# Optimization experiments

Measured on AMD Instinct MI355X. Metric: run time of the kernel, lower is better.

Reference implementation:

```python
import jax, jax.numpy as jnp
import numpy as np

N = 50000
E = 800000
IN_C = 128
HID = 64
HEADS = 4
OUT_C = 64
NEG_SLOPE = 0.2


def _glorot(key, shape):
    fan = shape[0] + shape[-1]
    return jax.random.normal(key, shape, dtype=jnp.float32) * jnp.sqrt(2.0 / fan)


def setup_inputs() -> dict:
    key = jax.random.key(0)
    ks = jax.random.split(key, 12)
    x = jax.random.normal(ks[0], (N, IN_C), dtype=jnp.float32)
    edge_index = jax.random.randint(ks[1], (2, E), 0, N, dtype=jnp.int64)
    edge_attr = jax.random.normal(ks[2], (E, 8), dtype=jnp.float32)
    # gat1: in -> heads*hid
    W1 = _glorot(ks[3], (IN_C, HEADS * HID))
    att_src1 = _glorot(ks[4], (HEADS, HID))
    att_dst1 = _glorot(ks[5], (HEADS, HID))
    b1 = jnp.zeros((HEADS * HID,), dtype=jnp.float32)
    # gat2: heads*hid -> out, 1 head
    W2 = _glorot(ks[6], (HEADS * HID, OUT_C))
    att_src2 = _glorot(ks[7], (1, OUT_C))
    att_dst2 = _glorot(ks[8], (1, OUT_C))
    b2 = jnp.zeros((OUT_C,), dtype=jnp.float32)
    return {"x": x, "edge_index": edge_index, "edge_attr": edge_attr,
            "W1": W1, "att_src1": att_src1, "att_dst1": att_dst1, "b1": b1,
            "W2": W2, "att_src2": att_src2, "att_dst2": att_dst2, "b2": b2}


def _gat_conv(x, src, dst, W, att_src, att_dst, b, heads, n_nodes):
    # x: [N, Cin] -> h: [N, H, C]
    h = (x @ W).reshape(n_nodes, heads, -1)
    a_src = jnp.sum(h * att_src, axis=-1)  # [N, H]
    a_dst = jnp.sum(h * att_dst, axis=-1)  # [N, H]
    e = jax.nn.leaky_relu(a_src[src] + a_dst[dst], NEG_SLOPE)  # [Etot, H]
    # segment softmax over destination node (self-loops guarantee non-empty segments)
    m = jax.ops.segment_max(e, dst, num_segments=n_nodes)      # [N, H]
    w = jnp.exp(e - m[dst])
    denom = jax.ops.segment_sum(w, dst, num_segments=n_nodes)  # [N, H]
    alpha = w / (denom[dst] + 1e-16)                           # [Etot, H]
    out = jax.ops.segment_sum(alpha[:, :, None] * h[src], dst, num_segments=n_nodes)
    return out.reshape(n_nodes, -1) + b  # concat heads (identity when heads==1)


def reference(x, edge_index, edge_attr, W1, att_src1, att_dst1, b1, W2, att_src2, att_dst2, b2):
    # PyG GATConv with edge_dim=None ignores edge_attr; add_self_loops=True by default.
    loop = jnp.arange(N, dtype=edge_index.dtype)
    src = jnp.concatenate([edge_index[0], loop])
    dst = jnp.concatenate([edge_index[1], loop])
    h = jax.nn.elu(_gat_conv(x, src, dst, W1, att_src1, att_dst1, b1, HEADS, N))
    out = jax.nn.elu(_gat_conv(h, src, dst, W2, att_src2, att_dst2, b2, 1, N))
    return out
```

## Files before the change

### kernel.cpp

```cpp
#include <hip/hip_runtime.h>
#include <hip/hip_bf16.h>
#include <math.h>

#define LEAKY 0.2f

#define BM 64
#define BN 64
#define BK 32
__global__ __launch_bounds__(256) void gemm_att(const float* __restrict__ A,
                                                const float* __restrict__ B,
                                                float* __restrict__ C,
                                                const float* __restrict__ att_s,
                                                const float* __restrict__ att_d,
                                                float* __restrict__ asrc,
                                                float* __restrict__ adst,
                                                int M, int K, int NC) {
    __shared__ float As[BK][BM + 1];
    __shared__ float Bs[BK][BN];
    const int tid = threadIdx.x;
    const int bm = blockIdx.x * BM;
    const int bn = blockIdx.y * BN;
    const int tx = tid & 15, ty = tid >> 4;
    float acc[4][4] = {};
    for (int k0 = 0; k0 < K; k0 += BK) {
        #pragma unroll
        for (int i = 0; i < (BM * BK) / 256; ++i) {
            int idx = tid + i * 256;
            int r = idx >> 5, c = idx & 31;
            int gr = bm + r;
            As[c][r] = (gr < M) ? A[(size_t)gr * K + k0 + c] : 0.f;
        }
        #pragma unroll
        for (int i = 0; i < (BK * BN) / 256; ++i) {
            int idx = tid + i * 256;
            int r = idx >> 6, c = idx & 63;
            Bs[r][c] = B[(size_t)(k0 + r) * NC + bn + c];
        }
        __syncthreads();
        #pragma unroll
        for (int k = 0; k < BK; ++k) {
            float a[4], b[4];
            #pragma unroll
            for (int i = 0; i < 4; ++i) a[i] = As[k][ty * 4 + i];
            #pragma unroll
            for (int j = 0; j < 4; ++j) b[j] = Bs[k][tx * 4 + j];
            #pragma unroll
            for (int i = 0; i < 4; ++i)
                #pragma unroll
                for (int j = 0; j < 4; ++j)
                    acc[i][j] += a[i] * b[j];
        }
        __syncthreads();
    }
    float s_att[4], d_att[4];
    #pragma unroll
    for (int j = 0; j < 4; ++j) {
        s_att[j] = att_s[bn + tx * 4 + j];
        d_att[j] = att_d[bn + tx * 4 + j];
    }
    const int head = bn >> 6;
    const int H = NC >> 6;
    #pragma unroll
    for (int i = 0; i < 4; ++i) {
        int gr = bm + ty * 4 + i;
        float ps = 0.f, pd = 0.f;
        #pragma unroll
        for (int j = 0; j < 4; ++j) {
            ps += acc[i][j] * s_att[j];
            pd += acc[i][j] * d_att[j];
        }
        #pragma unroll
        for (int o = 1; o < 16; o <<= 1) {
            ps += __shfl_xor(ps, o);
            pd += __shfl_xor(pd, o);
        }
        if (gr < M) {
            #pragma unroll
            for (int j = 0; j < 4; ++j)
                C[(size_t)gr * NC + bn + tx * 4 + j] = acc[i][j];
            if (tx == 0) {
                asrc[gr * H + head] = ps;
                adst[gr * H + head] = pd;
            }
        }
    }
}

__global__ __launch_bounds__(256) void count_deg(const int* __restrict__ ei, int E_, int N_,
                                                 int* __restrict__ deg) {
    int eid = blockIdx.x * 256 + threadIdx.x;
    int Etot = E_ + N_;
    if (eid >= Etot) return;
    int dst = (eid < E_) ? ei[E_ + eid] : (eid - E_);
    atomicAdd(&deg[dst], 1);
}

__global__ __launch_bounds__(1024) void scan_offsets(const int* __restrict__ deg,
                                                     int* __restrict__ off, int n) {
    __shared__ int wsum[16];
    int tid = threadIdx.x;
    int lane = tid & 63, w = tid >> 6;
    int chunk = (n + 1023) / 1024;
    int b = tid * chunk;
    int e = min(b + chunk, n);
    int s = 0;
    for (int i = b; i < e; ++i) s += deg[i];
    int v = s;
    #pragma unroll
    for (int o = 1; o < 64; o <<= 1) {
        int t = __shfl_up(v, o);
        if (lane >= o) v += t;
    }
    if (lane == 63) wsum[w] = v;
    __syncthreads();
    if (w == 0) {
        int t = (lane < 16) ? wsum[lane] : 0;
        #pragma unroll
        for (int o = 1; o < 16; o <<= 1) {
            int u = __shfl_up(t, o);
            if (lane >= o) t += u;
        }
        if (lane < 16) wsum[lane] = t;
    }
    __syncthreads();
    int acc = (w > 0 ? wsum[w - 1] : 0) + (v - s);
    for (int i = b; i < e; ++i) { off[i] = acc; acc += deg[i]; }
    if (e == n) off[n] = acc;
}

__global__ __launch_bounds__(256) void scatter_edges(const int* __restrict__ ei, int E_, int N_,
                                                     int* __restrict__ off,
                                                     int* __restrict__ csr) {
    int eid = blockIdx.x * 256 + threadIdx.x;
    int Etot = E_ + N_;
    if (eid >= Etot) return;
    int src, dst;
    if (eid < E_) { src = ei[eid]; dst = ei[E_ + eid]; }
    else          { src = dst = eid - E_; }
    int pos = atomicAdd(&off[dst], 1);
    csr[pos] = src;
}

__global__ __launch_bounds__(256) void gat_agg_h4(const int* __restrict__ off,
                                                  const int* __restrict__ csr,
                                                  const float* __restrict__ asrc,
                                                  const float* __restrict__ adst,
                                                  const float* __restrict__ hsrc,
                                                  const float* __restrict__ bias,
                                                  float* __restrict__ outp, int N_) {
    __shared__ float wls[4][256];
    __shared__ int   uls[4][64];
    int wv = threadIdx.x >> 6, lane = threadIdx.x & 63;
    int node = blockIdx.x * 4 + wv;
    if (node >= N_) return;
    int s = node ? off[node - 1] : 0;
    int e = off[node];
    int deg = e - s;
    float4 ad = *(const float4*)(adst + node * 4);
    float* wl = wls[wv];
    int*   ul = uls[wv];
    float a0 = 0.f, a1 = 0.f, a2 = 0.f, a3 = 0.f;
    float d0 = 0.f, d1 = 0.f, d2 = 0.f, d3 = 0.f;

    if (deg <= 64) {
        float e0 = -INFINITY, e1 = -INFINITY, e2 = -INFINITY, e3 = -INFINITY;
        int u = 0;
        if (lane < deg) {
            u = csr[s + lane];
            float4 as = *(const float4*)(asrc + u * 4);
            e0 = as.x + ad.x; e0 = e0 > 0.f ? e0 : LEAKY * e0;
            e1 = as.y + ad.y; e1 = e1 > 0.f ? e1 : LEAKY * e1;
            e2 = as.z + ad.z; e2 = e2 > 0.f ? e2 : LEAKY * e2;
            e3 = as.w + ad.w; e3 = e3 > 0.f ? e3 : LEAKY * e3;
        }
        float m0 = e0, m1 = e1, m2 = e2, m3 = e3;
        #pragma unroll
        for (int o = 32; o > 0; o >>= 1) {
            m0 = fmaxf(m0, __shfl_xor(m0, o));
            m1 = fmaxf(m1, __shfl_xor(m1, o));
            m2 = fmaxf(m2, __shfl_xor(m2, o));
            m3 = fmaxf(m3, __shfl_xor(m3, o));
        }
        if (lane < deg) {
            float w0 = __expf(e0 - m0), w1 = __expf(e1 - m1);
            float w2 = __expf(e2 - m2), w3 = __expf(e3 - m3);
            d0 = w0; d1 = w1; d2 = w2; d3 = w3;
            wl[lane] = w0; wl[64 + lane] = w1; wl[128 + lane] = w2; wl[192 + lane] = w3;
            ul[lane] = u;
        }
        int j = 0;
        for (; j + 2 <= deg; j += 2) {
            int u0 = ul[j], u1 = ul[j + 1];
            float W00 = wl[j],     W01 = wl[64 + j],     W02 = wl[128 + j],     W03 = wl[192 + j];
            float W10 = wl[j + 1], W11 = wl[64 + j + 1], W12 = wl[128 + j + 1], W13 = wl[192 + j + 1];
            const float* hp0 = hsrc + (size_t)u0 * 256 + lane;
            const float* hp1 = hsrc + (size_t)u1 * 256 + lane;
            float g00 = hp0[0], g01 = hp0[64], g02 = hp0[128], g03 = hp0[192];
            float g10 = hp1[0], g11 = hp1[64], g12 = hp1[128], g13 = hp1[192];
            a0 += W00 * g00; a1 += W01 * g01; a2 += W02 * g02; a3 += W03 * g03;
            a0 += W10 * g10; a1 += W11 * g11; a2 += W12 * g12; a3 += W13 * g13;
        }
        if (j < deg) {
            int u0 = ul[j];
            const float* hp = hsrc + (size_t)u0 * 256 + lane;
            a0 += wl[j] * hp[0];
            a1 += wl[64 + j] * hp[64];
            a2 += wl[128 + j] * hp[128];
            a3 += wl[192 + j] * hp[192];
        }
    } else {
        float m0 = -INFINITY, m1 = -INFINITY, m2 = -INFINITY, m3 = -INFINITY;
        for (int i = s + lane; i < e; i += 64) {
            int u = csr[i];
            float4 as = *(const float4*)(asrc + u * 4);
            float t;
            t = as.x + ad.x; t = t > 0.f ? t : LEAKY * t; m0 = fmaxf(m0, t);
            t = as.y + ad.y; t = t > 0.f ? t : LEAKY * t; m1 = fmaxf(m1, t);
            t = as.z + ad.z; t = t > 0.f ? t : LEAKY * t; m2 = fmaxf(m2, t);
            t = as.w + ad.w; t = t > 0.f ? t : LEAKY * t; m3 = fmaxf(m3, t);
        }
        #pragma unroll
        for (int o = 32; o > 0; o >>= 1) {
            m0 = fmaxf(m0, __shfl_xor(m0, o));
            m1 = fmaxf(m1, __shfl_xor(m1, o));
            m2 = fmaxf(m2, __shfl_xor(m2, o));
            m3 = fmaxf(m3, __shfl_xor(m3, o));
        }
        for (int base = s; base < e; base += 64) {
            int cnt = min(64, e - base);
            if (lane < cnt) {
                int u = csr[base + lane];
                float4 as = *(const float4*)(asrc + u * 4);
                float t, w;
                t = as.x + ad.x; t = t > 0.f ? t : LEAKY * t; w = __expf(t - m0); d0 += w; wl[lane] = w;
                t = as.y + ad.y; t = t > 0.f ? t : LEAKY * t; w = __expf(t - m1); d1 += w; wl[64 + lane] = w;
                t = as.z + ad.z; t = t > 0.f ? t : LEAKY * t; w = __expf(t - m2); d2 += w; wl[128 + lane] = w;
                t = as.w + ad.w; t = t > 0.f ? t : LEAKY * t; w = __expf(t - m3); d3 += w; wl[192 + lane] = w;
                ul[lane] = u;
            }
            for (int j = 0; j < cnt; ++j) {
                int u0 = ul[j];
                const float* hp = hsrc + (size_t)u0 * 256 + lane;
                a0 += wl[j] * hp[0];
                a1 += wl[64 + j] * hp[64];
                a2 += wl[128 + j] * hp[128];
                a3 += wl[192 + j] * hp[192];
            }
        }
    }
    #pragma unroll
    for (int o = 32; o > 0; o >>= 1) {
        d0 += __shfl_xor(d0, o);
        d1 += __shfl_xor(d1, o);
        d2 += __shfl_xor(d2, o);
        d3 += __shfl_xor(d3, o);
    }
    size_t ob = (size_t)node * 256 + lane;
    float v;
    v = a0 / (d0 + 1e-16f) + bias[lane];       outp[ob]       = v > 0.f ? v : expm1f(v);
    v = a1 / (d1 + 1e-16f) + bias[lane + 64];  outp[ob + 64]  = v > 0.f ? v : expm1f(v);
    v = a2 / (d2 + 1e-16f) + bias[lane + 128]; outp[ob + 128] = v > 0.f ? v : expm1f(v);
    v = a3 / (d3 + 1e-16f) + bias[lane + 192]; outp[ob + 192] = v > 0.f ? v : expm1f(v);
}

__global__ __launch_bounds__(256) void gat_agg_h1(const int* __restrict__ off,
                                                  const int* __restrict__ csr,
                                                  const float* __restrict__ asrc,
                                                  const float* __restrict__ adst,
                                                  const float* __restrict__ g,
                                                  const float* __restrict__ bias,
                                                  float* __restrict__ outp, int N_) {
    __shared__ float wls[4][64];
    __shared__ int   uls[4][64];
    int wv = threadIdx.x >> 6, lane = threadIdx.x & 63;
    int node = blockIdx.x * 4 + wv;
    if (node >= N_) return;
    int s = node ? off[node - 1] : 0;
    int e = off[node];
    int deg = e - s;
    float ad = adst[node];
    float* wl = wls[wv];
    int*   ul = uls[wv];
    float a = 0.f, d = 0.f;

    if (deg <= 64) {
        float ev = -INFINITY;
        int u = 0;
        if (lane < deg) {
            u = csr[s + lane];
            ev = asrc[u] + ad;
            ev = ev > 0.f ? ev : LEAKY * ev;
        }
        float mm = ev;
        #pragma unroll
        for (int o = 32; o > 0; o >>= 1) mm = fmaxf(mm, __shfl_xor(mm, o));
        if (lane < deg) {
            float w = __expf(ev - mm);
            d = w;
            wl[lane] = w;
            ul[lane] = u;
        }
        int j = 0;
        for (; j + 4 <= deg; j += 4) {
            int u0 = ul[j], u1 = ul[j + 1], u2 = ul[j + 2], u3 = ul[j + 3];
            float W0 = wl[j], W1 = wl[j + 1], W2 = wl[j + 2], W3 = wl[j + 3];
            float g0 = g[(size_t)u0 * 64 + lane];
            float g1 = g[(size_t)u1 * 64 + lane];
            float g2 = g[(size_t)u2 * 64 + lane];
            float g3 = g[(size_t)u3 * 64 + lane];
            a += W0 * g0; a += W1 * g1; a += W2 * g2; a += W3 * g3;
        }
        for (; j < deg; ++j) {
            a += wl[j] * g[(size_t)ul[j] * 64 + lane];
        }
    } else {
        float mm = -INFINITY;
        for (int i = s + lane; i < e; i += 64) {
            float t = asrc[csr[i]] + ad;
            t = t > 0.f ? t : LEAKY * t;
            mm = fmaxf(mm, t);
        }
        #pragma unroll
        for (int o = 32; o > 0; o >>= 1) mm = fmaxf(mm, __shfl_xor(mm, o));
        for (int base = s; base < e; base += 64) {
            int cnt = min(64, e - base);
            if (lane < cnt) {
                int u = csr[base + lane];
                float t = asrc[u] + ad;
                t = t > 0.f ? t : LEAKY * t;
                float w = __expf(t - mm);
                d += w;
                wl[lane] = w;
                ul[lane] = u;
            }
            for (int j = 0; j < cnt; ++j)
                a += wl[j] * g[(size_t)ul[j] * 64 + lane];
        }
    }
    #pragma unroll
    for (int o = 32; o > 0; o >>= 1) d += __shfl_xor(d, o);
    float v = a / (d + 1e-16f) + bias[lane];
    outp[(size_t)node * 64 + lane] = v > 0.f ? v : expm1f(v);
}

extern "C" void kernel_launch(void* const* d_in, const int* in_sizes, int n_in,
                              void* d_out, int out_size, void* d_ws, size_t ws_size,
                              hipStream_t stream) {
    const float* x        = (const float*)d_in[0];
    const int*   ei       = (const int*)d_in[1];
    const float* W1       = (const float*)d_in[3];
    const float* att_src1 = (const float*)d_in[4];
    const float* att_dst1 = (const float*)d_in[5];
    const float* b1       = (const float*)d_in[6];
    const float* W2       = (const float*)d_in[7];
    const float* att_src2 = (const float*)d_in[8];
    const float* att_dst2 = (const float*)d_in[9];
    const float* b2       = (const float*)d_in[10];
    float* out = (float*)d_out;

    const int N = in_sizes[0] / 128;
    const int E = in_sizes[1] / 2;
    const int Etot = E + N;

    float* ws    = (float*)d_ws;
    float* h1    = ws;
    float* h2    = h1 + (size_t)N * 256;
    float* g2    = h1;
    float* asrc1 = h2 + (size_t)N * 256;
    float* adst1 = asrc1 + (size_t)N * 4;
    float* asrc2 = adst1 + (size_t)N * 4;
    float* adst2 = asrc2 + N;
    int*   deg   = (int*)(adst2 + N);
    int*   off   = deg + (N + 1);
    int*   csr   = off + (N + 1);

    hipMemsetAsync(deg, 0, (N + 1) * sizeof(int), stream);
    count_deg<<<(Etot + 255) / 256, 256, 0, stream>>>(ei, E, N, deg);
    scan_offsets<<<1, 1024, 0, stream>>>(deg, off, N);
    scatter_edges<<<(Etot + 255) / 256, 256, 0, stream>>>(ei, E, N, off, csr);

    {
        dim3 g((N + BM - 1) / BM, 256 / BN);
        gemm_att<<<g, 256, 0, stream>>>(x, W1, h1, att_src1, att_dst1, asrc1, adst1, N, 128, 256);
    }
    gat_agg_h4<<<(N + 3) / 4, 256, 0, stream>>>(off, csr, asrc1, adst1, h1, b1, h2, N);

    {
        dim3 g((N + BM - 1) / BM, 64 / BN);
        gemm_att<<<g, 256, 0, stream>>>(h2, W2, g2, att_src2, att_dst2, asrc2, adst2, N, 256, 64);
    }
    gat_agg_h1<<<(N + 3) / 4, 256, 0, stream>>>(off, csr, asrc2, adst2, g2, b2, out, N);
}
```

Measured before the change: 573.9 us.

## Vectorize GAT aggregation gathers with float4 loads and edge-parallel sub-waves

In the 4-head aggregation kernel, each lane now owns four contiguous channels and gathers each neighbor row with a float4 load, picking its head weight from an interleaved shared-memory layout. The edge loop is unrolled by four to keep more gathers in flight. In the 1-head kernel, the wave splits into four 16-lane groups that each process a different neighbor with float4 loads, then combine partial sums with cross-lane shuffles. The aim is fewer, wider memory instructions and more memory-level parallelism in the gather-bound loops, at the cost of extra shuffle reductions and some idle lanes on the tail iterations.

After: 575.2 us. No clear change (+0.2%).

```diff
diff --git a/kernel.cpp b/kernel.cpp
--- a/kernel.cpp
+++ b/kernel.cpp
@@ -159,7 +159,9 @@
     float4 ad = *(const float4*)(adst + node * 4);
     float* wl = wls[wv];
     int*   ul = uls[wv];
-    float a0 = 0.f, a1 = 0.f, a2 = 0.f, a3 = 0.f;
+    const int hgrp = lane >> 4;
+    const float4* h4p = (const float4*)hsrc;
+    float4 acc = {0.f, 0.f, 0.f, 0.f};
     float d0 = 0.f, d1 = 0.f, d2 = 0.f, d3 = 0.f;
 
     if (deg <= 64) {
@@ -185,28 +187,30 @@
             float w0 = __expf(e0 - m0), w1 = __expf(e1 - m1);
             float w2 = __expf(e2 - m2), w3 = __expf(e3 - m3);
             d0 = w0; d1 = w1; d2 = w2; d3 = w3;
-            wl[lane] = w0; wl[64 + lane] = w1; wl[128 + lane] = w2; wl[192 + lane] = w3;
+            ((float4*)wl)[lane] = make_float4(w0, w1, w2, w3);
             ul[lane] = u;
         }
         int j = 0;
-        for (; j + 2 <= deg; j += 2) {
-            int u0 = ul[j], u1 = ul[j + 1];
-            float W00 = wl[j],     W01 = wl[64 + j],     W02 = wl[128 + j],     W03 = wl[192 + j];
-            float W10 = wl[j + 1], W11 = wl[64 + j + 1], W12 = wl[128 + j + 1], W13 = wl[192 + j + 1];
-            const float* hp0 = hsrc + (size_t)u0 * 256 + lane;
-            const float* hp1 = hsrc + (size_t)u1 * 256 + lane;
-            float g00 = hp0[0], g01 = hp0[64], g02 = hp0[128], g03 = hp0[192];
-            float g10 = hp1[0], g11 = hp1[64], g12 = hp1[128], g13 = hp1[192];
-            a0 += W00 * g00; a1 += W01 * g01; a2 += W02 * g02; a3 += W03 * g03;
-            a0 += W10 * g10; a1 += W11 * g11; a2 += W12 * g12; a3 += W13 * g13;
-        }
-        if (j < deg) {
+        for (; j + 4 <= deg; j += 4) {
+            int u0 = ul[j], u1 = ul[j + 1], u2 = ul[j + 2], u3 = ul[j + 3];
+            float W0 = wl[(j    ) * 4 + hgrp];
+            float W1 = wl[(j + 1) * 4 + hgrp];
+            float W2 = wl[(j + 2) * 4 + hgrp];
+            float W3 = wl[(j + 3) * 4 + hgrp];
+            float4 g0 = h4p[(size_t)u0 * 64 + lane];
+            float4 g1 = h4p[(size_t)u1 * 64 + lane];
+            float4 g2 = h4p[(size_t)u2 * 64 + lane];
+            float4 g3 = h4p[(size_t)u3 * 64 + lane];
+            acc.x += W0 * g0.x; acc.y += W0 * g0.y; acc.z += W0 * g0.z; acc.w += W0 * g0.w;
+            acc.x += W1 * g1.x; acc.y += W1 * g1.y; acc.z += W1 * g1.z; acc.w += W1 * g1.w;
+            acc.x += W2 * g2.x; acc.y += W2 * g2.y; acc.z += W2 * g2.z; acc.w += W2 * g2.w;
+            acc.x += W3 * g3.x; acc.y += W3 * g3.y; acc.z += W3 * g3.z; acc.w += W3 * g3.w;
+        }
+        for (; j < deg; ++j) {
             int u0 = ul[j];
-            const float* hp = hsrc + (size_t)u0 * 256 + lane;
-            a0 += wl[j] * hp[0];
-            a1 += wl[64 + j] * hp[64];
-            a2 += wl[128 + j] * hp[128];
-            a3 += wl[192 + j] * hp[192];
+            float W0 = wl[j * 4 + hgrp];
+            float4 g0 = h4p[(size_t)u0 * 64 + lane];
+            acc.x += W0 * g0.x; acc.y += W0 * g0.y; acc.z += W0 * g0.z; acc.w += W0 * g0.w;
         }
     } else {
         float m0 = -INFINITY, m1 = -INFINITY, m2 = -INFINITY, m3 = -INFINITY;
@@ -231,20 +235,35 @@
             if (lane < cnt) {
                 int u = csr[base + lane];
                 float4 as = *(const float4*)(asrc + u * 4);
-                float t, w;
-                t = as.x + ad.x; t = t > 0.f ? t : LEAKY * t; w = __expf(t - m0); d0 += w; wl[lane] = w;
-                t = as.y + ad.y; t = t > 0.f ? t : LEAKY * t; w = __expf(t - m1); d1 += w; wl[64 + lane] = w;
-                t = as.z + ad.z; t = t > 0.f ? t : LEAKY * t; w = __expf(t - m2); d2 += w; wl[128 + lane] = w;
-                t = as.w + ad.w; t = t > 0.f ? t : LEAKY * t; w = __expf(t - m3); d3 += w; wl[192 + lane] = w;
+                float t, w0, w1, w2, w3;
+                t = as.x + ad.x; t = t > 0.f ? t : LEAKY * t; w0 = __expf(t - m0); d0 += w0;
+                t = as.y + ad.y; t = t > 0.f ? t : LEAKY * t; w1 = __expf(t - m1); d1 += w1;
+                t = as.z + ad.z; t = t > 0.f ? t : LEAKY * t; w2 = __expf(t - m2); d2 += w2;
+                t = as.w + ad.w; t = t > 0.f ? t : LEAKY * t; w3 = __expf(t - m3); d3 += w3;
+                ((float4*)wl)[lane] = make_float4(w0, w1, w2, w3);
                 ul[lane] = u;
             }
-            for (int j = 0; j < cnt; ++j) {
+            int j = 0;
+            for (; j + 4 <= cnt; j += 4) {
+                int u0 = ul[j], u1 = ul[j + 1], u2 = ul[j + 2], u3 = ul[j + 3];
+                float W0 = wl[(j    ) * 4 + hgrp];
+                float W1 = wl[(j + 1) * 4 + hgrp];
+                float W2 = wl[(j + 2) * 4 + hgrp];
+                float W3 = wl[(j + 3) * 4 + hgrp];
+                float4 g0 = h4p[(size_t)u0 * 64 + lane];
+                float4 g1 = h4p[(size_t)u1 * 64 + lane];
+                float4 g2 = h4p[(size_t)u2 * 64 + lane];
+                float4 g3 = h4p[(size_t)u3 * 64 + lane];
+                acc.x += W0 * g0.x; acc.y += W0 * g0.y; acc.z += W0 * g0.z; acc.w += W0 * g0.w;
+                acc.x += W1 * g1.x; acc.y += W1 * g1.y; acc.z += W1 * g1.z; acc.w += W1 * g1.w;
+                acc.x += W2 * g2.x; acc.y += W2 * g2.y; acc.z += W2 * g2.z; acc.w += W2 * g2.w;
+                acc.x += W3 * g3.x; acc.y += W3 * g3.y; acc.z += W3 * g3.z; acc.w += W3 * g3.w;
+            }
+            for (; j < cnt; ++j) {
                 int u0 = ul[j];
-                const float* hp = hsrc + (size_t)u0 * 256 + lane;
-                a0 += wl[j] * hp[0];
-                a1 += wl[64 + j] * hp[64];
-                a2 += wl[128 + j] * hp[128];
-                a3 += wl[192 + j] * hp[192];
+                float W0 = wl[j * 4 + hgrp];
+                float4 g0 = h4p[(size_t)u0 * 64 + lane];
+                acc.x += W0 * g0.x; acc.y += W0 * g0.y; acc.z += W0 * g0.z; acc.w += W0 * g0.w;
             }
         }
     }
@@ -255,12 +274,15 @@
         d2 += __shfl_xor(d2, o);
         d3 += __shfl_xor(d3, o);
     }
-    size_t ob = (size_t)node * 256 + lane;
-    float v;
-    v = a0 / (d0 + 1e-16f) + bias[lane];       outp[ob]       = v > 0.f ? v : expm1f(v);
-    v = a1 / (d1 + 1e-16f) + bias[lane + 64];  outp[ob + 64]  = v > 0.f ? v : expm1f(v);
-    v = a2 / (d2 + 1e-16f) + bias[lane + 128]; outp[ob + 128] = v > 0.f ? v : expm1f(v);
-    v = a3 / (d3 + 1e-16f) + bias[lane + 192]; outp[ob + 192] = v > 0.f ? v : expm1f(v);
+    float dh = hgrp == 0 ? d0 : hgrp == 1 ? d1 : hgrp == 2 ? d2 : d3;
+    float rdh = 1.f / (dh + 1e-16f);
+    float4 bi = *(const float4*)(bias + lane * 4);
+    float4 v;
+    v.x = acc.x * rdh + bi.x; v.x = v.x > 0.f ? v.x : expm1f(v.x);
+    v.y = acc.y * rdh + bi.y; v.y = v.y > 0.f ? v.y : expm1f(v.y);
+    v.z = acc.z * rdh + bi.z; v.z = v.z > 0.f ? v.z : expm1f(v.z);
+    v.w = acc.w * rdh + bi.w; v.w = v.w > 0.f ? v.w : expm1f(v.w);
+    ((float4*)(outp + (size_t)node * 256))[lane] = v;
 }
 
 __global__ __launch_bounds__(256) void gat_agg_h1(const int* __restrict__ off,
@@ -281,7 +303,11 @@
     float ad = adst[node];
     float* wl = wls[wv];
     int*   ul = uls[wv];
-    float a = 0.f, d = 0.f;
+    const int sub = lane >> 4;
+    const int cl  = lane & 15;
+    const float4* g4 = (const float4*)g;
+    float4 acc = {0.f, 0.f, 0.f, 0.f};
+    float d = 0.f;
 
     if (deg <= 64) {
         float ev = -INFINITY;
@@ -301,17 +327,29 @@
             ul[lane] = u;
         }
         int j = 0;
+        for (; j + 16 <= deg; j += 16) {
+            int ua = ul[j + sub], ub = ul[j + 4 + sub], uc = ul[j + 8 + sub], ud = ul[j + 12 + sub];
+            float Wa = wl[j + sub], Wb = wl[j + 4 + sub], Wc = wl[j + 8 + sub], Wd = wl[j + 12 + sub];
+            float4 ga = g4[(size_t)ua * 16 + cl];
+            float4 gb = g4[(size_t)ub * 16 + cl];
+            float4 gc = g4[(size_t)uc * 16 + cl];
+            float4 gd = g4[(size_t)ud * 16 + cl];
+            acc.x += Wa * ga.x; acc.y += Wa * ga.y; acc.z += Wa * ga.z; acc.w += Wa * ga.w;
+            acc.x += Wb * gb.x; acc.y += Wb * gb.y; acc.z += Wb * gb.z; acc.w += Wb * gb.w;
+            acc.x += Wc * gc.x; acc.y += Wc * gc.y; acc.z += Wc * gc.z; acc.w += Wc * gc.w;
+            acc.x += Wd * gd.x; acc.y += Wd * gd.y; acc.z += Wd * gd.z; acc.w += Wd * gd.w;
+        }
         for (; j + 4 <= deg; j += 4) {
-            int u0 = ul[j], u1 = ul[j + 1], u2 = ul[j + 2], u3 = ul[j + 3];
-            float W0 = wl[j], W1 = wl[j + 1], W2 = wl[j + 2], W3 = wl[j + 3];
-            float g0 = g[(size_t)u0 * 64 + lane];
-            float g1 = g[(size_t)u1 * 64 + lane];
-            float g2 = g[(size_t)u2 * 64 + lane];
-            float g3 = g[(size_t)u3 * 64 + lane];
-            a += W0 * g0; a += W1 * g1; a += W2 * g2; a += W3 * g3;
-        }
-        for (; j < deg; ++j) {
-            a += wl[j] * g[(size_t)ul[j] * 64 + lane];
+            int ua = ul[j + sub];
+            float Wa = wl[j + sub];
+            float4 ga = g4[(size_t)ua * 16 + cl];
+            acc.x += Wa * ga.x; acc.y += Wa * ga.y; acc.z += Wa * ga.z; acc.w += Wa * ga.w;
+        }
+        if (sub < deg - j) {
+            int ua = ul[j + sub];
+            float Wa = wl[j + sub];
+            float4 ga = g4[(size_t)ua * 16 + cl];
+            acc.x += Wa * ga.x; acc.y += Wa * ga.y; acc.z += Wa * ga.z; acc.w += Wa * ga.w;
         }
     } else {
         float mm = -INFINITY;
@@ -333,14 +371,37 @@
                 wl[lane] = w;
                 ul[lane] = u;
             }
-            for (int j = 0; j < cnt; ++j)
-                a += wl[j] * g[(size_t)ul[j] * 64 + lane];
-        }
-    }
+            int j = 0;
+            for (; j + 4 <= cnt; j += 4) {
+                int ua = ul[j + sub];
+                float Wa = wl[j + sub];
+                float4 ga = g4[(size_t)ua * 16 + cl];
+                acc.x += Wa * ga.x; acc.y += Wa * ga.y; acc.z += Wa * ga.z; acc.w += Wa * ga.w;
+            }
+            if (sub < cnt - j) {
+                int ua = ul[j + sub];
+                float Wa = wl[j + sub];
+                float4 ga = g4[(size_t)ua * 16 + cl];
+                acc.x += Wa * ga.x; acc.y += Wa * ga.y; acc.z += Wa * ga.z; acc.w += Wa * ga.w;
+            }
+        }
+    }
+    acc.x += __shfl_xor(acc.x, 16); acc.x += __shfl_xor(acc.x, 32);
+    acc.y += __shfl_xor(acc.y, 16); acc.y += __shfl_xor(acc.y, 32);
+    acc.z += __shfl_xor(acc.z, 16); acc.z += __shfl_xor(acc.z, 32);
+    acc.w += __shfl_xor(acc.w, 16); acc.w += __shfl_xor(acc.w, 32);
     #pragma unroll
     for (int o = 32; o > 0; o >>= 1) d += __shfl_xor(d, o);
-    float v = a / (d + 1e-16f) + bias[lane];
-    outp[(size_t)node * 64 + lane] = v > 0.f ? v : expm1f(v);
+    if (sub == 0) {
+        float rd = 1.f / (d + 1e-16f);
+        float4 bi = ((const float4*)bias)[cl];
+        float4 v;
+        v.x = acc.x * rd + bi.x; v.x = v.x > 0.f ? v.x : expm1f(v.x);
+        v.y = acc.y * rd + bi.y; v.y = v.y > 0.f ? v.y : expm1f(v.y);
+        v.z = acc.z * rd + bi.z; v.z = v.z > 0.f ? v.z : expm1f(v.z);
+        v.w = acc.w * rd + bi.w; v.w = v.w > 0.f ? v.w : expm1f(v.w);
+        ((float4*)(outp + (size_t)node * 64))[cl] = v;
+    }
 }
 
 extern "C" void kernel_launch(void* const* d_in, const int* in_sizes, int n_in,
```
